# Performance work log

Measured on AMD Instinct MI355X. Metric: run time of the kernel, lower is better.

Reference implementation:

```python
import jax, jax.numpy as jnp
import numpy as np

DIM_INPUT = 8192
DIM_OUTPUT = 8192
N_FANOUT = 16
BATCH = 1024
WEIGHT = 100.0
NNZ = DIM_INPUT * N_FANOUT


def setup_inputs() -> dict:
    key = jax.random.key(0)
    rng = np.random.default_rng(0)
    # pre: each input neuron appears N_FANOUT times (arange % dim_input)
    pre = jnp.asarray(np.arange(NNZ) % DIM_INPUT, dtype=jnp.int32)
    # post: random permutation modulo dim_output (fixed random connectivity)
    post_np = rng.permutation(max(DIM_INPUT, DIM_OUTPUT) * N_FANOUT)[:NNZ] % DIM_OUTPUT
    post = jnp.asarray(post_np, dtype=jnp.int32)
    x = jax.random.normal(key, (BATCH, DIM_INPUT), dtype=jnp.float32)
    return {"x": x, "pre": pre, "post": post}


def reference(x, pre, post):
    # Sparse W (dim_output x dim_input) with W[post[e], pre[e]] += WEIGHT
    # (torch.sparse coalesces duplicates by summation; scatter-add matches).
    # y[b, j] = sum_{e: post[e]==j} WEIGHT * x[b, pre[e]]
    gathered = WEIGHT * jnp.take(x, pre, axis=1)          # [B, NNZ]
    y = jax.ops.segment_sum(gathered.T, post, num_segments=DIM_OUTPUT)  # [DIM_OUTPUT, B]
    return y.T                                             # [B, DIM_OUTPUT]
```

## Files before the change

kernel.cpp:

```cpp
#include <hip/hip_runtime.h>
#include <hip/hip_fp16.h>

#define DIM_IN   8192
#define DIM_OUT  8192
#define FAN      16
#define BATCH    1024
#define NNZ      (DIM_IN * FAN)
#define ROUT     32

__global__ __launch_bounds__(1024)
void build_scan_kernel(const int* __restrict__ pre,
                       const int* __restrict__ post,
                       int* __restrict__ idx) {
    __shared__ int cnt[ROUT];
    __shared__ int sidx[ROUT * FAN];
    const int t  = threadIdx.x;
    const int j0 = blockIdx.x * ROUT;

    if (t < ROUT) cnt[t] = 0;
    __syncthreads();

    for (int base = 0; base < NNZ; base += 4096) {
        const int e0 = base + t;
        const int p0 = post[e0];
        const int p1 = post[e0 + 1024];
        const int p2 = post[e0 + 2048];
        const int p3 = post[e0 + 3072];

        const unsigned r0 = (unsigned)(p0 - j0);
        const unsigned r1 = (unsigned)(p1 - j0);
        const unsigned r2 = (unsigned)(p2 - j0);
        const unsigned r3 = (unsigned)(p3 - j0);

        if (r0 < ROUT) { int s = atomicAdd(&cnt[r0], 1); if (s < FAN) sidx[r0 * FAN + s] = pre[e0]; }
        if (r1 < ROUT) { int s = atomicAdd(&cnt[r1], 1); if (s < FAN) sidx[r1 * FAN + s] = pre[e0 + 1024]; }
        if (r2 < ROUT) { int s = atomicAdd(&cnt[r2], 1); if (s < FAN) sidx[r2 * FAN + s] = pre[e0 + 2048]; }
        if (r3 < ROUT) { int s = atomicAdd(&cnt[r3], 1); if (s < FAN) sidx[r3 * FAN + s] = pre[e0 + 3072]; }
    }
    __syncthreads();

    if (t < ROUT * FAN) idx[(size_t)j0 * FAN + t] = sidx[t];
}

__global__ __launch_bounds__(256)
void transpose_kernel(const float* __restrict__ x, __half* __restrict__ xt) {
    const int t  = threadIdx.x;
    const int it = blockIdx.x & 127;
    const int bt = blockIdx.x >> 7;
    const int i0 = it * 64, b0 = bt * 64;
    const int bq = t & 15;
    const int iq = t >> 4;

    float4 m[4];
#pragma unroll
    for (int r = 0; r < 4; ++r)
        m[r] = *reinterpret_cast<const float4*>(
            x + (size_t)(b0 + bq * 4 + r) * DIM_IN + i0 + iq * 4);

#pragma unroll
    for (int e = 0; e < 4; ++e) {
        __half2 lo, hi;
        lo.x = __float2half(((const float*)&m[0])[e]);
        lo.y = __float2half(((const float*)&m[1])[e]);
        hi.x = __float2half(((const float*)&m[2])[e]);
        hi.y = __float2half(((const float*)&m[3])[e]);
        uint2 w;
        w.x = *reinterpret_cast<unsigned*>(&lo);
        w.y = *reinterpret_cast<unsigned*>(&hi);
        *reinterpret_cast<uint2*>(xt + (size_t)(i0 + iq * 4 + e) * BATCH + b0 + bq * 4) = w;
    }
}

#define JT 64
#define BT 256
__global__ __launch_bounds__(1024)
void spmm_kernel(const __half* __restrict__ xt,
                 const int*    __restrict__ idx,
                 float*        __restrict__ y) {
    __shared__ int sidx[JT * FAN];
    const int bid   = blockIdx.x;
    const int x8    = bid & 7;
    const int grp   = bid >> 3;
    const int btile = x8 >> 1;
    const int jtile = grp * 2 + (x8 & 1);
    const int j0 = jtile * JT;
    const int b0 = btile * BT;
    const int t  = threadIdx.x;

    sidx[t] = idx[(size_t)j0 * FAN + t];
    __syncthreads();

    const int jj = t >> 4;
    const int bb = t & 15;

    float acc[16];
#pragma unroll
    for (int m = 0; m < 16; ++m) acc[m] = 0.f;

    const __half* base = xt + b0 + bb * 16;
#pragma unroll
    for (int k = 0; k < FAN; ++k) {
        const int i = sidx[jj * FAN + k];
        const uint4* p = reinterpret_cast<const uint4*>(base + (size_t)i * BATCH);
        const uint4 u0 = p[0];
        const uint4 u1 = p[1];
        float2 f;
        f = __half22float2(*reinterpret_cast<const __half2*>(&u0.x)); acc[0]  += f.x; acc[1]  += f.y;
        f = __half22float2(*reinterpret_cast<const __half2*>(&u0.y)); acc[2]  += f.x; acc[3]  += f.y;
        f = __half22float2(*reinterpret_cast<const __half2*>(&u0.z)); acc[4]  += f.x; acc[5]  += f.y;
        f = __half22float2(*reinterpret_cast<const __half2*>(&u0.w)); acc[6]  += f.x; acc[7]  += f.y;
        f = __half22float2(*reinterpret_cast<const __half2*>(&u1.x)); acc[8]  += f.x; acc[9]  += f.y;
        f = __half22float2(*reinterpret_cast<const __half2*>(&u1.y)); acc[10] += f.x; acc[11] += f.y;
        f = __half22float2(*reinterpret_cast<const __half2*>(&u1.z)); acc[12] += f.x; acc[13] += f.y;
        f = __half22float2(*reinterpret_cast<const __half2*>(&u1.w)); acc[14] += f.x; acc[15] += f.y;
    }

    float* yb = y + (size_t)(b0 + bb * 16) * DIM_OUT + j0 + jj;
#pragma unroll
    for (int m = 0; m < 16; ++m)
        yb[(size_t)m * DIM_OUT] = 100.0f * acc[m];
}

#define ROWS     8
#define BLOCK    1024
#define OSPLIT   2
#define OCHUNK   (DIM_OUT / OSPLIT)
#define LDS_BYTES (DIM_IN * ROWS * 2)
__global__ __launch_bounds__(BLOCK, 1)
void gather_kernel(const float* __restrict__ x,
                   const int*   __restrict__ idx,
                   float*       __restrict__ y) {
    extern __shared__ __half ldsh[];
    const int t  = threadIdx.x;
    const int b0 = (blockIdx.x >> 1) * ROWS;
    const int j0 = (blockIdx.x & 1) * OCHUNK;

#pragma unroll
    for (int c = 0; c < DIM_IN / BLOCK; ++c) {
        const int i = t + c * BLOCK;
        uint4 w;
        __half2 h;
        h.x = __float2half(x[(size_t)(b0 + 0) * DIM_IN + i]);
        h.y = __float2half(x[(size_t)(b0 + 1) * DIM_IN + i]);
        w.x = *reinterpret_cast<unsigned*>(&h);
        h.x = __float2half(x[(size_t)(b0 + 2) * DIM_IN + i]);
        h.y = __float2half(x[(size_t)(b0 + 3) * DIM_IN + i]);
        w.y = *reinterpret_cast<unsigned*>(&h);
        h.x = __float2half(x[(size_t)(b0 + 4) * DIM_IN + i]);
        h.y = __float2half(x[(size_t)(b0 + 5) * DIM_IN + i]);
        w.z = *reinterpret_cast<unsigned*>(&h);
        h.x = __float2half(x[(size_t)(b0 + 6) * DIM_IN + i]);
        h.y = __float2half(x[(size_t)(b0 + 7) * DIM_IN + i]);
        w.w = *reinterpret_cast<unsigned*>(&h);
        *reinterpret_cast<uint4*>(&ldsh[(size_t)i * ROWS]) = w;
    }
    __syncthreads();

#pragma unroll
    for (int o = 0; o < OCHUNK / BLOCK; ++o) {
        const int j = j0 + t + o * BLOCK;
        const int4* ip = reinterpret_cast<const int4*>(idx + (size_t)j * FAN);
        int4 i0 = ip[0];
        int4 i1 = ip[1];
        int4 i2 = ip[2];
        int4 i3 = ip[3];

        float a0=0,a1=0,a2=0,a3=0,a4=0,a5=0,a6=0,a7=0;
        auto accum = [&](int i) {
            const uint4 u = *reinterpret_cast<const uint4*>(&ldsh[(size_t)i * ROWS]);
            float2 f;
            f = __half22float2(*reinterpret_cast<const __half2*>(&u.x)); a0 += f.x; a1 += f.y;
            f = __half22float2(*reinterpret_cast<const __half2*>(&u.y)); a2 += f.x; a3 += f.y;
            f = __half22float2(*reinterpret_cast<const __half2*>(&u.z)); a4 += f.x; a5 += f.y;
            f = __half22float2(*reinterpret_cast<const __half2*>(&u.w)); a6 += f.x; a7 += f.y;
        };
        accum(i0.x); accum(i0.y); accum(i0.z); accum(i0.w);
        accum(i1.x); accum(i1.y); accum(i1.z); accum(i1.w);
        accum(i2.x); accum(i2.y); accum(i2.z); accum(i2.w);
        accum(i3.x); accum(i3.y); accum(i3.z); accum(i3.w);

        y[(size_t)(b0 + 0) * DIM_OUT + j] = 100.0f * a0;
        y[(size_t)(b0 + 1) * DIM_OUT + j] = 100.0f * a1;
        y[(size_t)(b0 + 2) * DIM_OUT + j] = 100.0f * a2;
        y[(size_t)(b0 + 3) * DIM_OUT + j] = 100.0f * a3;
        y[(size_t)(b0 + 4) * DIM_OUT + j] = 100.0f * a4;
        y[(size_t)(b0 + 5) * DIM_OUT + j] = 100.0f * a5;
        y[(size_t)(b0 + 6) * DIM_OUT + j] = 100.0f * a6;
        y[(size_t)(b0 + 7) * DIM_OUT + j] = 100.0f * a7;
    }
}

extern "C" void kernel_launch(void* const* d_in, const int* in_sizes, int n_in,
                              void* d_out, int out_size, void* d_ws, size_t ws_size,
                              hipStream_t stream) {
    const float* x    = (const float*)d_in[0];
    const int*   pre  = (const int*)d_in[1];
    const int*   post = (const int*)d_in[2];
    float*       y    = (float*)d_out;

    const size_t xt_bytes  = (size_t)DIM_IN * BATCH * sizeof(__half);
    const size_t idx_bytes = (size_t)NNZ * sizeof(int);

    if (ws_size >= xt_bytes + idx_bytes) {
        __half* xt  = (__half*)d_ws;
        int*    idx = (int*)((char*)d_ws + xt_bytes);

        build_scan_kernel<<<DIM_OUT / ROUT, 1024, 0, stream>>>(pre, post, idx);
        transpose_kernel<<<(DIM_IN / 64) * (BATCH / 64), 256, 0, stream>>>(x, xt);
        spmm_kernel<<<(DIM_OUT / JT) * (BATCH / BT), 1024, 0, stream>>>(xt, idx, y);
    } else {
        int* idx = (int*)d_ws;
        hipFuncSetAttribute((const void*)gather_kernel,
                            hipFuncAttributeMaxDynamicSharedMemorySize, LDS_BYTES);
        build_scan_kernel<<<DIM_OUT / ROUT, 1024, 0, stream>>>(pre, post, idx);
        gather_kernel<<<(BATCH / ROWS) * OSPLIT, BLOCK, LDS_BYTES, stream>>>(x, idx, y);
    }
}
```

Before: 141.8 us.

## Rework spmm into smaller blocks with fp16 packed accumulation and nontemporal stores

```diff
diff --git a/kernel.cpp b/kernel.cpp
--- a/kernel.cpp
+++ b/kernel.cpp
@@ -71,54 +71,67 @@
     }
 }
 
-#define JT 64
-#define BT 256
-__global__ __launch_bounds__(1024)
-void spmm_kernel(const __half* __restrict__ xt,
-                 const int*    __restrict__ idx,
-                 float*        __restrict__ y) {
-    __shared__ int sidx[JT * FAN];
+#define JT3 32
+#define BT3 128
+__global__ __launch_bounds__(256, 6)
+void spmm3_kernel(const __half* __restrict__ xt,
+                  const int*    __restrict__ idx,
+                  float*        __restrict__ y) {
+    __shared__ int sidx[JT3 * FAN];
     const int bid   = blockIdx.x;
-    const int x8    = bid & 7;
-    const int grp   = bid >> 3;
-    const int btile = x8 >> 1;
-    const int jtile = grp * 2 + (x8 & 1);
-    const int j0 = jtile * JT;
-    const int b0 = btile * BT;
-    const int t  = threadIdx.x;
-
-    sidx[t] = idx[(size_t)j0 * FAN + t];
-    __syncthreads();
-
-    const int jj = t >> 4;
-    const int bb = t & 15;
-
-    float acc[16];
-#pragma unroll
-    for (int m = 0; m < 16; ++m) acc[m] = 0.f;
-
+    const int btile = bid & 7;
+    const int jtile = bid >> 3;
+    const int j0 = jtile * JT3;
+    const int b0 = btile * BT3;
+    const int t  = threadIdx.x;
+
+    sidx[t]       = idx[(size_t)j0 * FAN + t];
+    sidx[t + 256] = idx[(size_t)j0 * FAN + t + 256];
+    __syncthreads();
+
+    const int jj = t >> 3;
+    const int bb = t & 7;
     const __half* base = xt + b0 + bb * 16;
-#pragma unroll
-    for (int k = 0; k < FAN; ++k) {
-        const int i = sidx[jj * FAN + k];
-        const uint4* p = reinterpret_cast<const uint4*>(base + (size_t)i * BATCH);
-        const uint4 u0 = p[0];
-        const uint4 u1 = p[1];
-        float2 f;
-        f = __half22float2(*reinterpret_cast<const __half2*>(&u0.x)); acc[0]  += f.x; acc[1]  += f.y;
-        f = __half22float2(*reinterpret_cast<const __half2*>(&u0.y)); acc[2]  += f.x; acc[3]  += f.y;
-        f = __half22float2(*reinterpret_cast<const __half2*>(&u0.z)); acc[4]  += f.x; acc[5]  += f.y;
-        f = __half22float2(*reinterpret_cast<const __half2*>(&u0.w)); acc[6]  += f.x; acc[7]  += f.y;
-        f = __half22float2(*reinterpret_cast<const __half2*>(&u1.x)); acc[8]  += f.x; acc[9]  += f.y;
-        f = __half22float2(*reinterpret_cast<const __half2*>(&u1.y)); acc[10] += f.x; acc[11] += f.y;
-        f = __half22float2(*reinterpret_cast<const __half2*>(&u1.z)); acc[12] += f.x; acc[13] += f.y;
-        f = __half22float2(*reinterpret_cast<const __half2*>(&u1.w)); acc[14] += f.x; acc[15] += f.y;
+
+    const __half2 z = __float2half2_rn(0.f);
+    __half2 accP[8] = {z, z, z, z, z, z, z, z};
+    __half2 accQ[8] = {z, z, z, z, z, z, z, z};
+
+#pragma unroll
+    for (int r = 0; r < 4; ++r) {
+        uint4 u[8];
+#pragma unroll
+        for (int e = 0; e < 4; ++e) {
+            const int i = sidx[jj * FAN + r * 4 + e];
+            const uint4* p = reinterpret_cast<const uint4*>(base + (size_t)i * BATCH);
+            u[2 * e]     = p[0];
+            u[2 * e + 1] = p[1];
+        }
+#pragma unroll
+        for (int e = 0; e < 4; ++e) {
+#pragma unroll
+            for (int q = 0; q < 4; ++q) {
+                const __half2 lo = *reinterpret_cast<const __half2*>(&((const unsigned*)&u[2 * e])[q]);
+                const __half2 hi = *reinterpret_cast<const __half2*>(&((const unsigned*)&u[2 * e + 1])[q]);
+                if (r < 2) {
+                    accP[q]     = __hadd2(accP[q], lo);
+                    accP[q + 4] = __hadd2(accP[q + 4], hi);
+                } else {
+                    accQ[q]     = __hadd2(accQ[q], lo);
+                    accQ[q + 4] = __hadd2(accQ[q + 4], hi);
+                }
+            }
+        }
     }
 
     float* yb = y + (size_t)(b0 + bb * 16) * DIM_OUT + j0 + jj;
 #pragma unroll
-    for (int m = 0; m < 16; ++m)
-        yb[(size_t)m * DIM_OUT] = 100.0f * acc[m];
+    for (int m = 0; m < 16; ++m) {
+        const int h = m >> 1;
+        const float vP = (m & 1) ? __high2float(accP[h]) : __low2float(accP[h]);
+        const float vQ = (m & 1) ? __high2float(accQ[h]) : __low2float(accQ[h]);
+        __builtin_nontemporal_store(100.0f * (vP + vQ), &yb[(size_t)m * DIM_OUT]);
+    }
 }
 
 #define ROWS     8
@@ -207,7 +220,7 @@
 
         build_scan_kernel<<<DIM_OUT / ROUT, 1024, 0, stream>>>(pre, post, idx);
         transpose_kernel<<<(DIM_IN / 64) * (BATCH / 64), 256, 0, stream>>>(x, xt);
-        spmm_kernel<<<(DIM_OUT / JT) * (BATCH / BT), 1024, 0, stream>>>(xt, idx, y);
+        spmm3_kernel<<<(DIM_OUT / JT3) * (BATCH / BT3), 256, 0, stream>>>(xt, idx, y);
     } else {
         int* idx = (int*)d_ws;
         hipFuncSetAttribute((const void*)gather_kernel,
```

Result: faster. 134.2 us (-5.4%).
